# Kernel tuning notes

Measured on AMD Instinct MI355X. Metric: run time of the kernel, lower is better.

Reference implementation:

```python
import jax, jax.numpy as jnp
import numpy as np

B = 512
NODES_PER_GRAPH = 256
N = B * NODES_PER_GRAPH
IN_DIM = 128
HID = 128
PAD_VALUE = -10000.0


def setup_inputs() -> dict:
    key = jax.random.key(0)
    ks = jax.random.split(key, 10)
    inp = {
        "last_node_batch": jax.random.normal(ks[0], (B, IN_DIM), jnp.float32),
        "h": jax.random.normal(ks[1], (N, HID), jnp.float32),
        # NodeEmbed: Linear(in_dim, hidden_dim)
        "W_embed": jax.random.normal(ks[2], (IN_DIM, HID), jnp.float32) / np.sqrt(IN_DIM),
        "b_embed": jnp.zeros((HID,), jnp.float32),
        # Linear_3(2H, 2H, 2)
        "W1": jax.random.normal(ks[3], (2 * HID, 2 * HID), jnp.float32) / np.sqrt(2 * HID),
        "b1": jnp.zeros((2 * HID,), jnp.float32),
        "W2": jax.random.normal(ks[4], (2 * HID, 2 * HID), jnp.float32) / np.sqrt(2 * HID),
        "b2": jnp.zeros((2 * HID,), jnp.float32),
        "W3": jax.random.normal(ks[5], (2 * HID, 2), jnp.float32) / np.sqrt(2 * HID),
        "b3": jnp.zeros((2,), jnp.float32),
        # ragged batch encoded as sorted segment ids (graph id per node)
        "segment_ids": jnp.repeat(jnp.arange(B, dtype=jnp.int64), NODES_PER_GRAPH),
        "max_nodes": NODES_PER_GRAPH,
    }
    return inp


def reference(last_node_batch, h, W_embed, b_embed, W1, b1, W2, b2, W3, b3,
              segment_ids, max_nodes):
    n = h.shape[0]
    b = last_node_batch.shape[0]
    # per-graph node embed, broadcast to each node of its graph (repeat+cat loop)
    node_embed = last_node_batch @ W_embed + b_embed          # [B, H]
    bcast = node_embed[segment_ids]                           # [N, H]
    stack = jnp.concatenate([h, bcast], axis=1)               # [N, 2H]
    # Linear_3 MLP
    out = jnp.tanh(stack @ W1 + b1)
    out = jnp.tanh(out @ W2 + b2)
    edges = out @ W3 + b3                                     # [N, 2]
    # unbatch + pad_sequence(padding_value=-10000), then flatten(1, -1)
    counts = jax.ops.segment_sum(jnp.ones((n,), jnp.int32), segment_ids, num_segments=b)
    offsets = jnp.cumsum(counts) - counts                     # start index of each graph
    pos = jnp.arange(n) - offsets[segment_ids]                # position within graph
    padded = jnp.full((b, max_nodes, 2), PAD_VALUE, dtype=edges.dtype)
    padded = padded.at[segment_ids, pos].set(edges)
    return padded.reshape(b, max_nodes * 2)
```

## Files before the change

kernel.cpp:

```cpp
#include <hip/hip_runtime.h>


typedef __attribute__((ext_vector_type(8))) short s16x8;
typedef __attribute__((ext_vector_type(4))) float f32x4;

#define K2   256
#define KH   128
#define LDK  264

__device__ __forceinline__ float b2f(unsigned short u) {
  return __builtin_bit_cast(float, (unsigned int)u << 16);
}
__device__ __forceinline__ unsigned short f2b(float f) {
  unsigned int u = __builtin_bit_cast(unsigned int, f);
  u += 0x7fffu + ((u >> 16) & 1u);
  return (unsigned short)(u >> 16);
}
__device__ __forceinline__ float pade_tanh(float x) {
  float x2 = x * x;
  float x4 = x2 * x2;
  float num = x * (945.0f + 105.0f * x2 + x4);
  float den = __builtin_fmaf(15.0f, x4, __builtin_fmaf(420.0f, x2, 945.0f));
  float r = num * __builtin_amdgcn_rcpf(den);
  return __builtin_fmaxf(-1.0f, __builtin_fminf(1.0f, r));
}
__device__ __forceinline__ unsigned int probe_is16(const unsigned int* wraw,
                                                   int t) {
  unsigned int w = wraw[t];
  unsigned int e = (w >> 7) & 0xFFu;
  unsigned long long m = __ballot(e >= 96 && e < 128);
  return (__popcll(m) >= 32) ? 1u : 0u;
}

__global__ __launch_bounds__(256) void prep_pack(
    const void* __restrict__ W1, const void* __restrict__ W2,
    const void* __restrict__ Wemb,
    unsigned short* __restrict__ W1P, unsigned short* __restrict__ W2P,
    unsigned short* __restrict__ W1loT)
{
  __shared__ unsigned int flagLds;
  const int blk = blockIdx.x, t = threadIdx.x;
  if (t < 64) { unsigned int f = probe_is16((const unsigned int*)Wemb, t);
                if (t == 0) flagLds = f; }
  __syncthreads();
  const bool is16 = flagLds != 0u;

  if (blk < 96) {
    const void* S; unsigned short* D; int k0, n0, pk;
    if (blk < 32) { S = W1; D = W1P; pk = 2048;
                    k0 = (blk & 3) * 32; n0 = (blk >> 2) * 32; }
    else { int b = blk - 32; S = W2; D = W2P; pk = 4096;
           k0 = (b & 7) * 32; n0 = (b >> 3) * 32; }
    #pragma unroll
    for (int q = 0; q < 4; ++q) {
      int idx = t + 256 * q;
      int ln = idx & 31, lk = idx >> 5;
      int n = n0 + ln, k = k0 + lk;
      unsigned short v = is16 ? ((const unsigned short*)S)[k * K2 + n]
                              : f2b(((const float*)S)[k * K2 + n]);
      D[(n >> 4) * pk + (k >> 3) * 128 + (n & 15) * 8 + (k & 7)] = v;
    }
  } else {
    int b = blk - 96;
    int k0 = (b & 3) * 32, n0 = (b >> 2) * 32;
    #pragma unroll
    for (int q = 0; q < 4; ++q) {
      int idx = t + 256 * q;
      int ln = idx & 31, lk = idx >> 5;
      int n = n0 + ln, k = k0 + lk;
      unsigned short v = is16
          ? ((const unsigned short*)W1)[(KH + k) * K2 + n]
          : f2b(((const float*)W1)[(KH + k) * K2 + n]);
      W1loT[n * KH + k] = v;
    }
  }
}

__global__ __launch_bounds__(256, 4) void mlp_fused(
    const void* __restrict__ h,     const void* __restrict__ last,
    const void* __restrict__ Wemb,  const void* __restrict__ bemb,
    const void* __restrict__ b1,    const void* __restrict__ b2,
    const void* __restrict__ W3,    const void* __restrict__ b3,
    const unsigned short* __restrict__ W1P,
    const unsigned short* __restrict__ W2P,
    const unsigned short* __restrict__ W1loT,
    void* __restrict__ out)
{
  __shared__ __align__(16) unsigned short smA[64 * LDK];
  __shared__ __align__(16) float embf[KH];
  __shared__ float ebias[K2];
  __shared__ float headp[4][64][2];
  __shared__ unsigned int flagLds;

  const int t    = threadIdx.x;
  const int lane = t & 63, w = t >> 6;
  const int quad = lane >> 4, l16 = lane & 15;
  const int base = blockIdx.x * 64;
  const int g    = base >> 8;

  if (t < 64) { unsigned int f = probe_is16((const unsigned int*)Wemb, t);
                if (t == 0) flagLds = f; }
  __syncthreads();
  const bool is16 = flagLds != 0u;

  if (is16) {
    const uint4* hp = (const uint4*)h;
    #pragma unroll
    for (int i = 0; i < 4; ++i) {
      int id = t + 256 * i;
      int r = id >> 4, c = id & 15;
      *(uint4*)&smA[r * LDK + c * 8] = hp[(size_t)(base + r) * 16 + c];
    }
  } else {
    const float4* hf = (const float4*)h;
    #pragma unroll
    for (int i = 0; i < 8; ++i) {
      int id = t + 256 * i;
      int r = id >> 5, c = id & 31;
      float4 v = hf[(size_t)(base + r) * 32 + c];
      ushort4 u;
      u.x = f2b(v.x); u.y = f2b(v.y); u.z = f2b(v.z); u.w = f2b(v.w);
      *(ushort4*)&smA[r * LDK + c * 4] = u;
    }
  }
  if (t < KH) {
    float a0 = 0.f, a1 = 0.f, a2 = 0.f, a3 = 0.f;
    if (is16) {
      const unsigned short* lp = (const unsigned short*)last + g * KH;
      const unsigned short* wp = (const unsigned short*)Wemb;
      #pragma unroll 2
      for (int k = 0; k < KH; k += 4) {
        a0 += b2f(lp[k])     * b2f(wp[k * KH + t]);
        a1 += b2f(lp[k + 1]) * b2f(wp[(k + 1) * KH + t]);
        a2 += b2f(lp[k + 2]) * b2f(wp[(k + 2) * KH + t]);
        a3 += b2f(lp[k + 3]) * b2f(wp[(k + 3) * KH + t]);
      }
      embf[t] = b2f(((const unsigned short*)bemb)[t]) + (a0 + a1) + (a2 + a3);
    } else {
      const float* lp = (const float*)last + g * KH;
      const float* wp = (const float*)Wemb;
      #pragma unroll 2
      for (int k = 0; k < KH; k += 4) {
        a0 += lp[k]     * wp[k * KH + t];
        a1 += lp[k + 1] * wp[(k + 1) * KH + t];
        a2 += lp[k + 2] * wp[(k + 2) * KH + t];
        a3 += lp[k + 3] * wp[(k + 3) * KH + t];
      }
      embf[t] = ((const float*)bemb)[t] + (a0 + a1) + (a2 + a3);
    }
  }
  __syncthreads();

  {
    const int n = t;
    float e0 = 0.f, e1 = 0.f, e2 = 0.f, e3 = 0.f;
    const unsigned short* wrow = W1loT + n * KH;
    #pragma unroll 4
    for (int k8 = 0; k8 < KH; k8 += 8) {
      s16x8 wv = *(const s16x8*)&wrow[k8];
      float4 ea = *(const float4*)&embf[k8];
      float4 eb = *(const float4*)&embf[k8 + 4];
      e0 += ea.x * b2f((unsigned short)wv[0]);
      e1 += ea.y * b2f((unsigned short)wv[1]);
      e2 += ea.z * b2f((unsigned short)wv[2]);
      e3 += ea.w * b2f((unsigned short)wv[3]);
      e0 += eb.x * b2f((unsigned short)wv[4]);
      e1 += eb.y * b2f((unsigned short)wv[5]);
      e2 += eb.z * b2f((unsigned short)wv[6]);
      e3 += eb.w * b2f((unsigned short)wv[7]);
    }
    float bb = is16 ? b2f(((const unsigned short*)b1)[n])
                    : ((const float*)b1)[n];
    ebias[n] = bb + (e0 + e1) + (e2 + e3);
  }

  f32x4 acc[4][4];
  #pragma unroll
  for (int i = 0; i < 4; ++i)
    #pragma unroll
    for (int c = 0; c < 4; ++c) acc[i][c] = f32x4{0.f, 0.f, 0.f, 0.f};
  #pragma unroll
  for (int kk = 0; kk < 4; ++kk) {
    s16x8 a[4], b[4];
    #pragma unroll
    for (int i = 0; i < 4; ++i)
      a[i] = *(const s16x8*)&smA[(i * 16 + l16) * LDK + kk * 32 + quad * 8];
    #pragma unroll
    for (int c = 0; c < 4; ++c)
      b[c] = *(const s16x8*)&W1P[(w * 4 + c) * 2048
                                 + (kk * 4 + quad) * 128 + l16 * 8];
    #pragma unroll
    for (int i = 0; i < 4; ++i)
      #pragma unroll
      for (int c = 0; c < 4; ++c)
        acc[i][c] = __builtin_amdgcn_mfma_f32_16x16x32_bf16(
            a[i], b[c], acc[i][c], 0, 0, 0);
  }
  __syncthreads();
  #pragma unroll
  for (int c = 0; c < 4; ++c) {
    int col = w * 64 + c * 16 + l16;
    float eb = ebias[col];
    #pragma unroll
    for (int i = 0; i < 4; ++i)
      #pragma unroll
      for (int rg = 0; rg < 4; ++rg)
        smA[(i * 16 + quad * 4 + rg) * LDK + col] =
            f2b(pade_tanh(acc[i][c][rg] + eb));
  }
  __syncthreads();

  #pragma unroll
  for (int i = 0; i < 4; ++i)
    #pragma unroll
    for (int c = 0; c < 4; ++c) acc[i][c] = f32x4{0.f, 0.f, 0.f, 0.f};
  #pragma unroll 2
  for (int kk = 0; kk < 8; ++kk) {
    s16x8 a[4], b[4];
    #pragma unroll
    for (int i = 0; i < 4; ++i)
      a[i] = *(const s16x8*)&smA[(i * 16 + l16) * LDK + kk * 32 + quad * 8];
    #pragma unroll
    for (int c = 0; c < 4; ++c)
      b[c] = *(const s16x8*)&W2P[(w * 4 + c) * 4096
                                 + (kk * 4 + quad) * 128 + l16 * 8];
    #pragma unroll
    for (int i = 0; i < 4; ++i)
      #pragma unroll
      for (int c = 0; c < 4; ++c)
        acc[i][c] = __builtin_amdgcn_mfma_f32_16x16x32_bf16(
            a[i], b[c], acc[i][c], 0, 0, 0);
  }
  __syncthreads();
  #pragma unroll
  for (int c = 0; c < 4; ++c) {
    int col = w * 64 + c * 16 + l16;
    float bb = is16 ? b2f(((const unsigned short*)b2)[col])
                    : ((const float*)b2)[col];
    #pragma unroll
    for (int i = 0; i < 4; ++i)
      #pragma unroll
      for (int rg = 0; rg < 4; ++rg)
        smA[(i * 16 + quad * 4 + rg) * LDK + col] =
            f2b(pade_tanh(acc[i][c][rg] + bb));
  }
  __syncthreads();

  {
    f32x4 accH[4];
    #pragma unroll
    for (int i = 0; i < 4; ++i) accH[i] = f32x4{0.f, 0.f, 0.f, 0.f};
    #pragma unroll
    for (int s = 0; s < 2; ++s) {
      int kk = 2 * w + s;
      s16x8 bh;
      if (is16) {
        const unsigned short* w3u = (const unsigned short*)W3;
        #pragma unroll
        for (int j = 0; j < 8; ++j)
          bh[j] = (short)w3u[(kk * 32 + quad * 8 + j) * 2 + (l16 & 1)];
      } else {
        const float* w3f = (const float*)W3;
        #pragma unroll
        for (int j = 0; j < 8; ++j)
          bh[j] = (short)f2b(w3f[(kk * 32 + quad * 8 + j) * 2 + (l16 & 1)]);
      }
      #pragma unroll
      for (int i = 0; i < 4; ++i) {
        s16x8 a = *(const s16x8*)&smA[(i * 16 + l16) * LDK
                                      + kk * 32 + quad * 8];
        accH[i] = __builtin_amdgcn_mfma_f32_16x16x32_bf16(
            a, bh, accH[i], 0, 0, 0);
      }
    }
    if (l16 < 2) {
      #pragma unroll
      for (int i = 0; i < 4; ++i)
        #pragma unroll
        for (int rg = 0; rg < 4; ++rg)
          headp[w][i * 16 + quad * 4 + rg][l16] = accH[i][rg];
    }
  }
  __syncthreads();
  if (t < 128) {
    const int r = t >> 1, e = t & 1;
    float b3e = is16 ? b2f(((const unsigned short*)b3)[e])
                     : ((const float*)b3)[e];
    float s = b3e + headp[0][r][e] + headp[1][r][e]
                  + headp[2][r][e] + headp[3][r][e];
    size_t idx = (size_t)(base + r) * 2 + e;
    if (is16) ((unsigned short*)out)[idx] = f2b(s);
    else      ((float*)out)[idx] = s;
  }
}

extern "C" void kernel_launch(void* const* d_in, const int* in_sizes, int n_in,
                              void* d_out, int out_size, void* d_ws, size_t ws_size,
                              hipStream_t stream) {
  (void)in_sizes; (void)n_in; (void)out_size; (void)ws_size;
  const void* last = d_in[0];
  const void* h    = d_in[1];
  const void* Wemb = d_in[2];
  const void* bemb = d_in[3];
  const void* W1   = d_in[4];
  const void* b1   = d_in[5];
  const void* W2   = d_in[6];
  const void* b2   = d_in[7];
  const void* W3   = d_in[8];
  const void* b3   = d_in[9];

  char* ws = (char*)d_ws;
  unsigned short* W1P   = (unsigned short*)(ws);
  unsigned short* W2P   = (unsigned short*)(ws + 65536);
  unsigned short* W1loT = (unsigned short*)(ws + 196608);

  prep_pack<<<dim3(128), dim3(256), 0, stream>>>(W1, W2, Wemb, W1P, W2P, W1loT);
  mlp_fused<<<dim3(2048), dim3(256), 0, stream>>>(
      h, last, Wemb, bemb, b1, b2, W3, b3, W1P, W2P, W1loT, d_out);
}
```

Before: 175.6 us.

## Process one graph per block, reuse embed and W1 fragments across four node tiles

The fused MLP kernel now runs one block per graph (512 blocks) and loops over four 64-row tiles of that graph. The per-graph node embedding and its projection through the lower half of W1 are computed once per block instead of once per 64-row tile, and that projection now uses MFMA on a packed W1lo layout. W1 fragments, W3 fragments and biases are held in registers across tiles, and the next tile's h rows are prefetched into registers while the current tile is processed. The costs are higher register pressure (launch bounds drop to 2 blocks per SM), fewer blocks to spread across the GPU, and the embedding is rounded to bf16 before the MFMA projection.

```diff
diff --git a/kernel.cpp b/kernel.cpp
--- a/kernel.cpp
+++ b/kernel.cpp
@@ -36,7 +36,7 @@
     const void* __restrict__ W1, const void* __restrict__ W2,
     const void* __restrict__ Wemb,
     unsigned short* __restrict__ W1P, unsigned short* __restrict__ W2P,
-    unsigned short* __restrict__ W1loT)
+    unsigned short* __restrict__ W1loP)
 {
   __shared__ unsigned int flagLds;
   const int blk = blockIdx.x, t = threadIdx.x;
@@ -45,49 +45,38 @@
   __syncthreads();
   const bool is16 = flagLds != 0u;
 
-  if (blk < 96) {
-    const void* S; unsigned short* D; int k0, n0, pk;
-    if (blk < 32) { S = W1; D = W1P; pk = 2048;
-                    k0 = (blk & 3) * 32; n0 = (blk >> 2) * 32; }
-    else { int b = blk - 32; S = W2; D = W2P; pk = 4096;
-           k0 = (b & 7) * 32; n0 = (b >> 3) * 32; }
-    #pragma unroll
-    for (int q = 0; q < 4; ++q) {
-      int idx = t + 256 * q;
-      int ln = idx & 31, lk = idx >> 5;
-      int n = n0 + ln, k = k0 + lk;
-      unsigned short v = is16 ? ((const unsigned short*)S)[k * K2 + n]
-                              : f2b(((const float*)S)[k * K2 + n]);
-      D[(n >> 4) * pk + (k >> 3) * 128 + (n & 15) * 8 + (k & 7)] = v;
-    }
-  } else {
-    int b = blk - 96;
-    int k0 = (b & 3) * 32, n0 = (b >> 2) * 32;
-    #pragma unroll
-    for (int q = 0; q < 4; ++q) {
-      int idx = t + 256 * q;
-      int ln = idx & 31, lk = idx >> 5;
-      int n = n0 + ln, k = k0 + lk;
-      unsigned short v = is16
-          ? ((const unsigned short*)W1)[(KH + k) * K2 + n]
-          : f2b(((const float*)W1)[(KH + k) * K2 + n]);
-      W1loT[n * KH + k] = v;
-    }
-  }
-}
-
-__global__ __launch_bounds__(256, 4) void mlp_fused(
+  const void* S; unsigned short* D; int k0, n0, pk, krow;
+  if (blk < 32) { S = W1; D = W1P; pk = 2048; krow = 0;
+                  k0 = (blk & 3) * 32; n0 = (blk >> 2) * 32; }
+  else if (blk < 96) { int b = blk - 32; S = W2; D = W2P; pk = 4096; krow = 0;
+                       k0 = (b & 7) * 32; n0 = (b >> 3) * 32; }
+  else { int b = blk - 96; S = W1; D = W1loP; pk = 2048; krow = KH;
+         k0 = (b & 3) * 32; n0 = (b >> 2) * 32; }
+  #pragma unroll
+  for (int q = 0; q < 4; ++q) {
+    int idx = t + 256 * q;
+    int ln = idx & 31, lk = idx >> 5;
+    int n = n0 + ln, k = k0 + lk;
+    unsigned short v = is16
+        ? ((const unsigned short*)S)[(krow + k) * K2 + n]
+        : f2b(((const float*)S)[(krow + k) * K2 + n]);
+    D[(n >> 4) * pk + (k >> 3) * 128 + (n & 15) * 8 + (k & 7)] = v;
+  }
+}
+
+__global__ __launch_bounds__(256, 2) void mlp_graph(
     const void* __restrict__ h,     const void* __restrict__ last,
     const void* __restrict__ Wemb,  const void* __restrict__ bemb,
     const void* __restrict__ b1,    const void* __restrict__ b2,
     const void* __restrict__ W3,    const void* __restrict__ b3,
     const unsigned short* __restrict__ W1P,
     const unsigned short* __restrict__ W2P,
-    const unsigned short* __restrict__ W1loT,
+    const unsigned short* __restrict__ W1loP,
     void* __restrict__ out)
 {
   __shared__ __align__(16) unsigned short smA[64 * LDK];
-  __shared__ __align__(16) float embf[KH];
+  __shared__ float embp[2][KH];
+  __shared__ __align__(16) unsigned short embb[KH];
   __shared__ float ebias[K2];
   __shared__ float headp[4][64][2];
   __shared__ unsigned int flagLds;
@@ -95,202 +84,239 @@
   const int t    = threadIdx.x;
   const int lane = t & 63, w = t >> 6;
   const int quad = lane >> 4, l16 = lane & 15;
-  const int base = blockIdx.x * 64;
-  const int g    = base >> 8;
+  const int g    = blockIdx.x;
 
   if (t < 64) { unsigned int f = probe_is16((const unsigned int*)Wemb, t);
                 if (t == 0) flagLds = f; }
   __syncthreads();
   const bool is16 = flagLds != 0u;
 
-  if (is16) {
-    const uint4* hp = (const uint4*)h;
-    #pragma unroll
-    for (int i = 0; i < 4; ++i) {
-      int id = t + 256 * i;
-      int r = id >> 4, c = id & 15;
-      *(uint4*)&smA[r * LDK + c * 8] = hp[(size_t)(base + r) * 16 + c];
-    }
-  } else {
-    const float4* hf = (const float4*)h;
-    #pragma unroll
-    for (int i = 0; i < 8; ++i) {
-      int id = t + 256 * i;
-      int r = id >> 5, c = id & 31;
-      float4 v = hf[(size_t)(base + r) * 32 + c];
-      ushort4 u;
-      u.x = f2b(v.x); u.y = f2b(v.y); u.z = f2b(v.z); u.w = f2b(v.w);
-      *(ushort4*)&smA[r * LDK + c * 4] = u;
-    }
-  }
-  if (t < KH) {
+  {
+    const int j = t & 127, half = t >> 7, k0 = half * 64;
     float a0 = 0.f, a1 = 0.f, a2 = 0.f, a3 = 0.f;
     if (is16) {
       const unsigned short* lp = (const unsigned short*)last + g * KH;
       const unsigned short* wp = (const unsigned short*)Wemb;
-      #pragma unroll 2
-      for (int k = 0; k < KH; k += 4) {
-        a0 += b2f(lp[k])     * b2f(wp[k * KH + t]);
-        a1 += b2f(lp[k + 1]) * b2f(wp[(k + 1) * KH + t]);
-        a2 += b2f(lp[k + 2]) * b2f(wp[(k + 2) * KH + t]);
-        a3 += b2f(lp[k + 3]) * b2f(wp[(k + 3) * KH + t]);
-      }
-      embf[t] = b2f(((const unsigned short*)bemb)[t]) + (a0 + a1) + (a2 + a3);
+      #pragma unroll 4
+      for (int k = k0; k < k0 + 64; k += 4) {
+        a0 += b2f(lp[k])     * b2f(wp[k * KH + j]);
+        a1 += b2f(lp[k + 1]) * b2f(wp[(k + 1) * KH + j]);
+        a2 += b2f(lp[k + 2]) * b2f(wp[(k + 2) * KH + j]);
+        a3 += b2f(lp[k + 3]) * b2f(wp[(k + 3) * KH + j]);
+      }
     } else {
       const float* lp = (const float*)last + g * KH;
       const float* wp = (const float*)Wemb;
-      #pragma unroll 2
-      for (int k = 0; k < KH; k += 4) {
-        a0 += lp[k]     * wp[k * KH + t];
-        a1 += lp[k + 1] * wp[(k + 1) * KH + t];
-        a2 += lp[k + 2] * wp[(k + 2) * KH + t];
-        a3 += lp[k + 3] * wp[(k + 3) * KH + t];
-      }
-      embf[t] = ((const float*)bemb)[t] + (a0 + a1) + (a2 + a3);
-    }
-  }
-  __syncthreads();
-
-  {
-    const int n = t;
-    float e0 = 0.f, e1 = 0.f, e2 = 0.f, e3 = 0.f;
-    const unsigned short* wrow = W1loT + n * KH;
-    #pragma unroll 4
-    for (int k8 = 0; k8 < KH; k8 += 8) {
-      s16x8 wv = *(const s16x8*)&wrow[k8];
-      float4 ea = *(const float4*)&embf[k8];
-      float4 eb = *(const float4*)&embf[k8 + 4];
-      e0 += ea.x * b2f((unsigned short)wv[0]);
-      e1 += ea.y * b2f((unsigned short)wv[1]);
-      e2 += ea.z * b2f((unsigned short)wv[2]);
-      e3 += ea.w * b2f((unsigned short)wv[3]);
-      e0 += eb.x * b2f((unsigned short)wv[4]);
-      e1 += eb.y * b2f((unsigned short)wv[5]);
-      e2 += eb.z * b2f((unsigned short)wv[6]);
-      e3 += eb.w * b2f((unsigned short)wv[7]);
-    }
-    float bb = is16 ? b2f(((const unsigned short*)b1)[n])
-                    : ((const float*)b1)[n];
-    ebias[n] = bb + (e0 + e1) + (e2 + e3);
-  }
-
-  f32x4 acc[4][4];
+      #pragma unroll 4
+      for (int k = k0; k < k0 + 64; k += 4) {
+        a0 += lp[k]     * wp[k * KH + j];
+        a1 += lp[k + 1] * wp[(k + 1) * KH + j];
+        a2 += lp[k + 2] * wp[(k + 2) * KH + j];
+        a3 += lp[k + 3] * wp[(k + 3) * KH + j];
+      }
+    }
+    embp[half][j] = (a0 + a1) + (a2 + a3);
+  }
+
+  s16x8 w1f[16];
   #pragma unroll
-  for (int i = 0; i < 4; ++i)
-    #pragma unroll
-    for (int c = 0; c < 4; ++c) acc[i][c] = f32x4{0.f, 0.f, 0.f, 0.f};
+  for (int kk = 0; kk < 4; ++kk)
+    #pragma unroll
+    for (int c = 0; c < 4; ++c)
+      w1f[kk * 4 + c] = *(const s16x8*)&W1P[(w * 4 + c) * 2048
+                                            + (kk * 4 + quad) * 128 + l16 * 8];
+  s16x8 bh[2];
   #pragma unroll
-  for (int kk = 0; kk < 4; ++kk) {
-    s16x8 a[4], b[4];
-    #pragma unroll
-    for (int i = 0; i < 4; ++i)
-      a[i] = *(const s16x8*)&smA[(i * 16 + l16) * LDK + kk * 32 + quad * 8];
-    #pragma unroll
-    for (int c = 0; c < 4; ++c)
-      b[c] = *(const s16x8*)&W1P[(w * 4 + c) * 2048
-                                 + (kk * 4 + quad) * 128 + l16 * 8];
-    #pragma unroll
-    for (int i = 0; i < 4; ++i)
-      #pragma unroll
-      for (int c = 0; c < 4; ++c)
-        acc[i][c] = __builtin_amdgcn_mfma_f32_16x16x32_bf16(
-            a[i], b[c], acc[i][c], 0, 0, 0);
-  }
-  __syncthreads();
+  for (int s = 0; s < 2; ++s) {
+    int kk = 2 * w + s;
+    #pragma unroll
+    for (int j = 0; j < 8; ++j) {
+      int kidx = (kk * 32 + quad * 8 + j) * 2 + (l16 & 1);
+      bh[s][j] = is16 ? (short)((const unsigned short*)W3)[kidx]
+                      : (short)f2b(((const float*)W3)[kidx]);
+    }
+  }
+  float b2v[4];
   #pragma unroll
   for (int c = 0; c < 4; ++c) {
     int col = w * 64 + c * 16 + l16;
-    float eb = ebias[col];
+    b2v[c] = is16 ? b2f(((const unsigned short*)b2)[col])
+                  : ((const float*)b2)[col];
+  }
+  float b3e = 0.f;
+  if (t < 128)
+    b3e = is16 ? b2f(((const unsigned short*)b3)[t & 1])
+               : ((const float*)b3)[t & 1];
+  __syncthreads();
+
+  if (t < KH) {
+    float e = is16 ? b2f(((const unsigned short*)bemb)[t])
+                   : ((const float*)bemb)[t];
+    embb[t] = f2b(e + embp[0][t] + embp[1][t]);
+  }
+  __syncthreads();
+
+  {
+    f32x4 eacc[4];
+    #pragma unroll
+    for (int c = 0; c < 4; ++c) eacc[c] = f32x4{0.f, 0.f, 0.f, 0.f};
+    #pragma unroll
+    for (int kk = 0; kk < 4; ++kk) {
+      s16x8 a = *(const s16x8*)&embb[kk * 32 + quad * 8];
+      #pragma unroll
+      for (int c = 0; c < 4; ++c) {
+        s16x8 b = *(const s16x8*)&W1loP[(w * 4 + c) * 2048
+                                        + (kk * 4 + quad) * 128 + l16 * 8];
+        eacc[c] = __builtin_amdgcn_mfma_f32_16x16x32_bf16(a, b, eacc[c],
+                                                          0, 0, 0);
+      }
+    }
+    if (quad == 0) {
+      #pragma unroll
+      for (int c = 0; c < 4; ++c) {
+        int col = w * 64 + c * 16 + l16;
+        float bb = is16 ? b2f(((const unsigned short*)b1)[col])
+                        : ((const float*)b1)[col];
+        ebias[col] = bb + eacc[c][0];
+      }
+    }
+  }
+
+  uint4 hreg[4];
+  const int pr = t >> 4, pc = t & 15;
+  auto load_tile = [&](int tile) {
+    int rbase = g * 256 + tile * 64;
+    if (is16) {
+      const uint4* hp = (const uint4*)h;
+      #pragma unroll
+      for (int i = 0; i < 4; ++i)
+        hreg[i] = hp[(size_t)(rbase + pr + 16 * i) * 16 + pc];
+    } else {
+      const float4* hf = (const float4*)h;
+      #pragma unroll
+      for (int i = 0; i < 4; ++i) {
+        float4 va = hf[(size_t)(rbase + pr + 16 * i) * 32 + pc * 2];
+        float4 vb = hf[(size_t)(rbase + pr + 16 * i) * 32 + pc * 2 + 1];
+        ushort4 ua, ub;
+        ua.x = f2b(va.x); ua.y = f2b(va.y); ua.z = f2b(va.z); ua.w = f2b(va.w);
+        ub.x = f2b(vb.x); ub.y = f2b(vb.y); ub.z = f2b(vb.z); ub.w = f2b(vb.w);
+        hreg[i] = make_uint4(
+            (unsigned)ua.x | ((unsigned)ua.y << 16),
+            (unsigned)ua.z | ((unsigned)ua.w << 16),
+            (unsigned)ub.x | ((unsigned)ub.y << 16),
+            (unsigned)ub.z | ((unsigned)ub.w << 16));
+      }
+    }
+  };
+  load_tile(0);
+
+  f32x4 acc[4][4];
+  for (int tile = 0; tile < 4; ++tile) {
+    const int base = g * 256 + tile * 64;
+    __syncthreads();
     #pragma unroll
     for (int i = 0; i < 4; ++i)
-      #pragma unroll
-      for (int rg = 0; rg < 4; ++rg)
-        smA[(i * 16 + quad * 4 + rg) * LDK + col] =
-            f2b(pade_tanh(acc[i][c][rg] + eb));
-  }
-  __syncthreads();
-
-  #pragma unroll
-  for (int i = 0; i < 4; ++i)
-    #pragma unroll
-    for (int c = 0; c < 4; ++c) acc[i][c] = f32x4{0.f, 0.f, 0.f, 0.f};
-  #pragma unroll 2
-  for (int kk = 0; kk < 8; ++kk) {
-    s16x8 a[4], b[4];
+      *(uint4*)&smA[(pr + 16 * i) * LDK + pc * 8] = hreg[i];
+    if (tile < 3) load_tile(tile + 1);
+    __syncthreads();
+
     #pragma unroll
     for (int i = 0; i < 4; ++i)
-      a[i] = *(const s16x8*)&smA[(i * 16 + l16) * LDK + kk * 32 + quad * 8];
-    #pragma unroll
-    for (int c = 0; c < 4; ++c)
-      b[c] = *(const s16x8*)&W2P[(w * 4 + c) * 4096
-                                 + (kk * 4 + quad) * 128 + l16 * 8];
+      #pragma unroll
+      for (int c = 0; c < 4; ++c) acc[i][c] = f32x4{0.f, 0.f, 0.f, 0.f};
+    #pragma unroll
+    for (int kk = 0; kk < 4; ++kk) {
+      s16x8 a[4];
+      #pragma unroll
+      for (int i = 0; i < 4; ++i)
+        a[i] = *(const s16x8*)&smA[(i * 16 + l16) * LDK + kk * 32 + quad * 8];
+      #pragma unroll
+      for (int i = 0; i < 4; ++i)
+        #pragma unroll
+        for (int c = 0; c < 4; ++c)
+          acc[i][c] = __builtin_amdgcn_mfma_f32_16x16x32_bf16(
+              a[i], w1f[kk * 4 + c], acc[i][c], 0, 0, 0);
+    }
+    __syncthreads();
+    #pragma unroll
+    for (int c = 0; c < 4; ++c) {
+      int col = w * 64 + c * 16 + l16;
+      float eb = ebias[col];
+      #pragma unroll
+      for (int i = 0; i < 4; ++i)
+        #pragma unroll
+        for (int rg = 0; rg < 4; ++rg)
+          smA[(i * 16 + quad * 4 + rg) * LDK + col] =
+              f2b(pade_tanh(acc[i][c][rg] + eb));
+    }
+    __syncthreads();
+
     #pragma unroll
     for (int i = 0; i < 4; ++i)
       #pragma unroll
+      for (int c = 0; c < 4; ++c) acc[i][c] = f32x4{0.f, 0.f, 0.f, 0.f};
+    #pragma unroll 2
+    for (int kk = 0; kk < 8; ++kk) {
+      s16x8 a[4], b[4];
+      #pragma unroll
+      for (int i = 0; i < 4; ++i)
+        a[i] = *(const s16x8*)&smA[(i * 16 + l16) * LDK + kk * 32 + quad * 8];
+      #pragma unroll
       for (int c = 0; c < 4; ++c)
-        acc[i][c] = __builtin_amdgcn_mfma_f32_16x16x32_bf16(
-            a[i], b[c], acc[i][c], 0, 0, 0);
-  }
-  __syncthreads();
-  #pragma unroll
-  for (int c = 0; c < 4; ++c) {
-    int col = w * 64 + c * 16 + l16;
-    float bb = is16 ? b2f(((const unsigned short*)b2)[col])
-                    : ((const float*)b2)[col];
-    #pragma unroll
-    for (int i = 0; i < 4; ++i)
-      #pragma unroll
-      for (int rg = 0; rg < 4; ++rg)
-        smA[(i * 16 + quad * 4 + rg) * LDK + col] =
-            f2b(pade_tanh(acc[i][c][rg] + bb));
-  }
-  __syncthreads();
-
-  {
-    f32x4 accH[4];
-    #pragma unroll
-    for (int i = 0; i < 4; ++i) accH[i] = f32x4{0.f, 0.f, 0.f, 0.f};
-    #pragma unroll
-    for (int s = 0; s < 2; ++s) {
-      int kk = 2 * w + s;
-      s16x8 bh;
-      if (is16) {
-        const unsigned short* w3u = (const unsigned short*)W3;
-        #pragma unroll
-        for (int j = 0; j < 8; ++j)
-          bh[j] = (short)w3u[(kk * 32 + quad * 8 + j) * 2 + (l16 & 1)];
-      } else {
-        const float* w3f = (const float*)W3;
-        #pragma unroll
-        for (int j = 0; j < 8; ++j)
-          bh[j] = (short)f2b(w3f[(kk * 32 + quad * 8 + j) * 2 + (l16 & 1)]);
-      }
-      #pragma unroll
-      for (int i = 0; i < 4; ++i) {
-        s16x8 a = *(const s16x8*)&smA[(i * 16 + l16) * LDK
-                                      + kk * 32 + quad * 8];
-        accH[i] = __builtin_amdgcn_mfma_f32_16x16x32_bf16(
-            a, bh, accH[i], 0, 0, 0);
-      }
-    }
-    if (l16 < 2) {
+        b[c] = *(const s16x8*)&W2P[(w * 4 + c) * 4096
+                                   + (kk * 4 + quad) * 128 + l16 * 8];
+      #pragma unroll
+      for (int i = 0; i < 4; ++i)
+        #pragma unroll
+        for (int c = 0; c < 4; ++c)
+          acc[i][c] = __builtin_amdgcn_mfma_f32_16x16x32_bf16(
+              a[i], b[c], acc[i][c], 0, 0, 0);
+    }
+    __syncthreads();
+    #pragma unroll
+    for (int c = 0; c < 4; ++c) {
+      int col = w * 64 + c * 16 + l16;
       #pragma unroll
       for (int i = 0; i < 4; ++i)
         #pragma unroll
         for (int rg = 0; rg < 4; ++rg)
-          headp[w][i * 16 + quad * 4 + rg][l16] = accH[i][rg];
-    }
-  }
-  __syncthreads();
-  if (t < 128) {
-    const int r = t >> 1, e = t & 1;
-    float b3e = is16 ? b2f(((const unsigned short*)b3)[e])
-                     : ((const float*)b3)[e];
-    float s = b3e + headp[0][r][e] + headp[1][r][e]
-                  + headp[2][r][e] + headp[3][r][e];
-    size_t idx = (size_t)(base + r) * 2 + e;
-    if (is16) ((unsigned short*)out)[idx] = f2b(s);
-    else      ((float*)out)[idx] = s;
+          smA[(i * 16 + quad * 4 + rg) * LDK + col] =
+              f2b(pade_tanh(acc[i][c][rg] + b2v[c]));
+    }
+    __syncthreads();
+
+    {
+      f32x4 accH[4];
+      #pragma unroll
+      for (int i = 0; i < 4; ++i) accH[i] = f32x4{0.f, 0.f, 0.f, 0.f};
+      #pragma unroll
+      for (int s = 0; s < 2; ++s) {
+        int kk = 2 * w + s;
+        #pragma unroll
+        for (int i = 0; i < 4; ++i) {
+          s16x8 a = *(const s16x8*)&smA[(i * 16 + l16) * LDK
+                                        + kk * 32 + quad * 8];
+          accH[i] = __builtin_amdgcn_mfma_f32_16x16x32_bf16(
+              a, bh[s], accH[i], 0, 0, 0);
+        }
+      }
+      if (l16 < 2) {
+        #pragma unroll
+        for (int i = 0; i < 4; ++i)
+          #pragma unroll
+          for (int rg = 0; rg < 4; ++rg)
+            headp[w][i * 16 + quad * 4 + rg][l16] = accH[i][rg];
+      }
+    }
+    __syncthreads();
+    if (t < 128) {
+      const int r = t >> 1, e = t & 1;
+      float s = b3e + headp[0][r][e] + headp[1][r][e]
+                    + headp[2][r][e] + headp[3][r][e];
+      size_t idx = (size_t)(base + r) * 2 + e;
+      if (is16) ((unsigned short*)out)[idx] = f2b(s);
+      else      ((float*)out)[idx] = s;
+    }
   }
 }
 
@@ -312,9 +338,9 @@
   char* ws = (char*)d_ws;
   unsigned short* W1P   = (unsigned short*)(ws);
   unsigned short* W2P   = (unsigned short*)(ws + 65536);
-  unsigned short* W1loT = (unsigned short*)(ws + 196608);
-
-  prep_pack<<<dim3(128), dim3(256), 0, stream>>>(W1, W2, Wemb, W1P, W2P, W1loT);
-  mlp_fused<<<dim3(2048), dim3(256), 0, stream>>>(
-      h, last, Wemb, bemb, b1, b2, W3, b3, W1P, W2P, W1loT, d_out);
-}
+  unsigned short* W1loP = (unsigned short*)(ws + 196608);
+
+  prep_pack<<<dim3(128), dim3(256), 0, stream>>>(W1, W2, Wemb, W1P, W2P, W1loP);
+  mlp_graph<<<dim3(512), dim3(256), 0, stream>>>(
+      h, last, Wemb, bemb, b1, b2, W3, b3, W1P, W2P, W1loP, d_out);
+}
```

Result: faster. 161.0 us (-8.3%).
